# Optimization experiments

Measured on AMD Instinct MI355X. Metric: run time of the kernel, lower is better.

The kernel has to match this reference:

```python
import jax, jax.numpy as jnp
import numpy as np

B, U, I, H = 1024, 8, 512, 512


def setup_inputs() -> dict:
    key = jax.random.key(0)
    ks = jax.random.split(key, 6)
    s_i = 1.0 / np.sqrt(H)  # torch GRU init: U(-1/sqrt(H), 1/sqrt(H))
    inputs = jax.random.normal(ks[0], (B, U, I), dtype=jnp.float32)
    hidden = jax.random.normal(ks[1], (B, U, H), dtype=jnp.float32)
    W_ih = jax.random.uniform(ks[2], (U, 3 * H, I), minval=-s_i, maxval=s_i, dtype=jnp.float32)
    W_hh = jax.random.uniform(ks[3], (U, 3 * H, H), minval=-s_i, maxval=s_i, dtype=jnp.float32)
    b_ih = jax.random.uniform(ks[4], (U, 3 * H), minval=-s_i, maxval=s_i, dtype=jnp.float32)
    b_hh = jax.random.uniform(ks[5], (U, 3 * H), minval=-s_i, maxval=s_i, dtype=jnp.float32)
    return {"inputs": inputs, "hidden": hidden, "W_ih": W_ih, "W_hh": W_hh, "b_ih": b_ih, "b_hh": b_hh}


def reference(inputs, hidden, W_ih, W_hh, b_ih, b_hh):
    # Grouped single-step GRU: all num_units cells computed in one batched matmul pair.
    # gx, gh: [B, U, 3H]
    gx = jnp.einsum('bui,ugi->bug', inputs, W_ih) + b_ih[None]
    gh = jnp.einsum('buh,ugh->bug', hidden, W_hh) + b_hh[None]
    xr, xz, xn = jnp.split(gx, 3, axis=-1)
    hr, hz, hn = jnp.split(gh, 3, axis=-1)
    r = jax.nn.sigmoid(xr + hr)
    z = jax.nn.sigmoid(xz + hz)
    n = jnp.tanh(xn + r * hn)
    return (1.0 - z) * n + z * hidden
```

## Files before the change

### kernel.cpp

```cpp
#include <hip/hip_runtime.h>
#include <hip/hip_bf16.h>
#include <stdint.h>


#define B_ 1024
#define U_ 8
#define I_ 512
#define H_ 512
#define KDIM 512

#define NX (B_ * U_ * I_)
#define NW (U_ * 3 * H_ * I_)
#define OFF_X 0
#define OFF_H NX
#define OFF_WIH (2 * NX)
#define OFF_WHH (2 * NX + NW)
#define NTOT (2 * NX + 2 * NW)
#define WS_NEED ((size_t)NTOT * 2)

#define BM 64
#define BN 64
#define BK 32
#define NITER (KDIM / BK)
#define SLAB_B 4096
#define BUF_B (8 * SLAB_B)
#define ESTR 68

typedef __attribute__((ext_vector_type(8))) short short8;
typedef __attribute__((ext_vector_type(4))) float floatx4;

__device__ __forceinline__ unsigned int pk2bf(float a, float b) {
    float2 f2; f2.x = a; f2.y = b;
    union { __hip_bfloat162 h; unsigned int u; } cv;
    cv.h = __float22bfloat162_rn(f2);
    return cv.u;
}

__device__ __forceinline__ void async16(const void* g, void* l) {
    __builtin_amdgcn_global_load_lds(
        (const __attribute__((address_space(1))) void*)g,
        (__attribute__((address_space(3))) void*)l, 16, 0, 0);
}

__global__ __launch_bounds__(256)
void convert_bf16_kernel(const float* __restrict__ x, const float* __restrict__ h,
                         const float* __restrict__ wih, const float* __restrict__ whh,
                         unsigned short* __restrict__ ws)
{
    const size_t base = ((size_t)blockIdx.x * 256 + threadIdx.x) * 8;
    const float* src; size_t off;
    if (base < (size_t)OFF_H)        { src = x;   off = OFF_X; }
    else if (base < (size_t)OFF_WIH) { src = h;   off = OFF_H; }
    else if (base < (size_t)OFF_WHH) { src = wih; off = OFF_WIH; }
    else                             { src = whh; off = OFF_WHH; }
    const float4 v0 = *(const float4*)(src + (base - off));
    const float4 v1 = *(const float4*)(src + (base - off) + 4);
    uint4 o;
    o.x = pk2bf(v0.x, v0.y);
    o.y = pk2bf(v0.z, v0.w);
    o.z = pk2bf(v1.x, v1.y);
    o.w = pk2bf(v1.z, v1.w);
    *(uint4*)(ws + base) = o;
}

union Smem {
    char raw[2 * BUF_B];
    float ep[3][BM * ESTR];
};

__global__ __launch_bounds__(512, 4)
void gru_main_kernel(const unsigned short* __restrict__ ws,
                     const float* __restrict__ hidden,
                     const float* __restrict__ b_ih,
                     const float* __restrict__ b_hh,
                     float* __restrict__ out)
{
    const int u  = blockIdx.x >> 3;
    const int nb = blockIdx.x & 7;
    const int mb = blockIdx.y;
    const int b0 = mb * BM;
    const int h0 = nb * BN;

    const int tid  = threadIdx.x;
    const int lane = tid & 63;
    const int wave = tid >> 6;
    const int lr   = lane & 15;
    const int q    = lane >> 4;
    const int wm   = wave & 1;
    const int wn   = (wave >> 1) & 1;
    const int g2   = wave >> 2;

    __shared__ Smem smem;

    const unsigned short* gbase; int grstr;
    if (wave == 0)      { gbase = ws + OFF_X + ((size_t)b0 * U_ + u) * I_; grstr = U_ * I_; }
    else if (wave == 1) { gbase = ws + OFF_H + ((size_t)b0 * U_ + u) * H_; grstr = U_ * H_; }
    else if (wave <= 4) { int g = wave - 2; gbase = ws + OFF_WIH + ((size_t)(u * 3 + g) * H_ + h0) * I_; grstr = I_; }
    else                { int g = wave - 5; gbase = ws + OFF_WHH + ((size_t)(u * 3 + g) * H_ + h0) * H_; grstr = H_; }

    const unsigned short* gptr[4];
    int ldsoff[4];
    #pragma unroll
    for (int i = 0; i < 4; ++i) {
        const int line = i * 8 + (lane >> 3);
        const int pos  = (lane & 7) ^ (line & 7);
        const int row  = 2 * line + (pos >> 2);
        const int ch   = pos & 3;
        gptr[i]   = gbase + (size_t)row * grstr + ch * 8;
        ldsoff[i] = wave * SLAB_B + i * 1024 + lane * 16;
    }

    int aoff[2], boff[2];
    #pragma unroll
    for (int t = 0; t < 2; ++t) {
        {
            const int r = wm * 32 + t * 16 + lr;
            const int line = r >> 1;
            const int pp = (((r & 1) * 4 + q)) ^ (line & 7);
            aoff[t] = line * 128 + pp * 16;
        }
        {
            const int r = wn * 32 + t * 16 + lr;
            const int line = r >> 1;
            const int pp = (((r & 1) * 4 + q)) ^ (line & 7);
            boff[t] = line * 128 + pp * 16;
        }
    }

    floatx4 acc[3][2][2];
    #pragma unroll
    for (int g = 0; g < 3; ++g)
        #pragma unroll
        for (int mt = 0; mt < 2; ++mt)
            #pragma unroll
            for (int nt = 0; nt < 2; ++nt)
                acc[g][mt][nt] = (floatx4){0.f, 0.f, 0.f, 0.f};

    const int aslab = g2;
    const int bbase = 2 + 3 * g2;

    #pragma unroll
    for (int i = 0; i < 4; ++i) {
        async16(gptr[i], smem.raw + ldsoff[i]);
        gptr[i] += BK;
    }

    for (int it = 0; it < NITER; ++it) {
        const int cur = it & 1;
        __syncthreads();

        if (it + 1 < NITER) {
            const int nxtoff = ((it + 1) & 1) * BUF_B;
            #pragma unroll
            for (int i = 0; i < 4; ++i) {
                async16(gptr[i], smem.raw + nxtoff + ldsoff[i]);
                gptr[i] += BK;
            }
        }

        const char* base = smem.raw + cur * BUF_B;
        const short8 a0 = *(const short8*)(base + aslab * SLAB_B + aoff[0]);
        const short8 a1 = *(const short8*)(base + aslab * SLAB_B + aoff[1]);
        #pragma unroll
        for (int g = 0; g < 3; ++g) {
            const char* bslab = base + (bbase + g) * SLAB_B;
            #pragma unroll
            for (int nt = 0; nt < 2; ++nt) {
                const short8 bf = *(const short8*)(bslab + boff[nt]);
                acc[g][0][nt] = __builtin_amdgcn_mfma_f32_16x16x32_bf16(a0, bf, acc[g][0][nt], 0, 0, 0);
                acc[g][1][nt] = __builtin_amdgcn_mfma_f32_16x16x32_bf16(a1, bf, acc[g][1][nt], 0, 0, 0);
            }
        }
    }
    __syncthreads();

    const float* bih = b_ih + u * (3 * H_);
    const float* bhh = b_hh + u * (3 * H_);

    if (g2 == 1) {
        #pragma unroll
        for (int nt = 0; nt < 2; ++nt) {
            const int col = wn * 32 + nt * 16 + lr;
            const float bhr = bhh[h0 + col];
            const float bhz = bhh[H_ + h0 + col];
            const float bhn = bhh[2 * H_ + h0 + col];
            #pragma unroll
            for (int mt = 0; mt < 2; ++mt)
                #pragma unroll
                for (int r = 0; r < 4; ++r) {
                    const int row = wm * 32 + mt * 16 + q * 4 + r;
                    smem.ep[0][row * ESTR + col] = acc[0][mt][nt][r] + bhr;
                    smem.ep[1][row * ESTR + col] = acc[1][mt][nt][r] + bhz;
                    smem.ep[2][row * ESTR + col] = acc[2][mt][nt][r] + bhn;
                }
        }
    }
    __syncthreads();

    if (g2 == 0) {
        #pragma unroll
        for (int nt = 0; nt < 2; ++nt) {
            const int col  = wn * 32 + nt * 16 + lr;
            const int hcol = h0 + col;
            const float bir  = bih[hcol];
            const float biz  = bih[H_ + hcol];
            const float bin_ = bih[2 * H_ + hcol];
            #pragma unroll
            for (int mt = 0; mt < 2; ++mt)
                #pragma unroll
                for (int r = 0; r < 4; ++r) {
                    const int row  = wm * 32 + mt * 16 + q * 4 + r;
                    const size_t gidx = ((size_t)(b0 + row) * U_ + u) * H_ + hcol;
                    const float hprev = hidden[gidx];
                    const float hr = smem.ep[0][row * ESTR + col];
                    const float hz = smem.ep[1][row * ESTR + col];
                    const float hn = smem.ep[2][row * ESTR + col];
                    const float xr = acc[0][mt][nt][r] + bir;
                    const float xz = acc[1][mt][nt][r] + biz;
                    const float xn = acc[2][mt][nt][r] + bin_;
                    const float rg = 1.f / (1.f + __expf(-(xr + hr)));
                    const float zg = 1.f / (1.f + __expf(-(xz + hz)));
                    const float ng = tanhf(xn + rg * hn);
                    out[gidx] = (1.f - zg) * ng + zg * hprev;
                }
        }
    }
}

#define LSTR 40
union SmemF {
    short bf[8][BM * LSTR];
    float ep[3][BM * ESTR];
};

__global__ __launch_bounds__(512, 4)
void gru_fallback_kernel(const float* __restrict__ inputs, const float* __restrict__ hidden,
                         const float* __restrict__ W_ih, const float* __restrict__ W_hh,
                         const float* __restrict__ b_ih, const float* __restrict__ b_hh,
                         float* __restrict__ out)
{
    const int nb = blockIdx.x;
    const int mb = blockIdx.y;
    const int u  = blockIdx.z;
    const int b0 = mb * BM, h0 = nb * BN;
    const int tid = threadIdx.x, lane = tid & 63, wave = tid >> 6;
    const int lr = lane & 15, q = lane >> 4;
    const int wm = wave & 1, wn = (wave >> 1) & 1, g2 = wave >> 2;

    __shared__ SmemF smem;

    const float* srcs[8]; int rstr[8];
    srcs[0] = inputs + ((size_t)b0 * U_ + u) * I_;         rstr[0] = U_ * I_;
    srcs[1] = hidden + ((size_t)b0 * U_ + u) * H_;         rstr[1] = U_ * H_;
    srcs[2] = W_ih + ((size_t)(u * 3 + 0) * H_ + h0) * I_; rstr[2] = I_;
    srcs[3] = W_ih + ((size_t)(u * 3 + 1) * H_ + h0) * I_; rstr[3] = I_;
    srcs[4] = W_ih + ((size_t)(u * 3 + 2) * H_ + h0) * I_; rstr[4] = I_;
    srcs[5] = W_hh + ((size_t)(u * 3 + 0) * H_ + h0) * H_; rstr[5] = H_;
    srcs[6] = W_hh + ((size_t)(u * 3 + 1) * H_ + h0) * H_; rstr[6] = H_;
    srcs[7] = W_hh + ((size_t)(u * 3 + 2) * H_ + h0) * H_; rstr[7] = H_;

    const int srow = tid >> 3, c4 = (tid & 7) * 4;
    const float* tb[8];
    #pragma unroll
    for (int s = 0; s < 8; ++s) tb[s] = srcs[s] + (size_t)srow * rstr[s] + c4;

    floatx4 acc[3][2][2];
    #pragma unroll
    for (int g = 0; g < 3; ++g)
        #pragma unroll
        for (int mt = 0; mt < 2; ++mt)
            #pragma unroll
            for (int nt = 0; nt < 2; ++nt) acc[g][mt][nt] = (floatx4){0.f, 0.f, 0.f, 0.f};

    const int aslab = g2, bbase = 2 + 3 * g2;
    float4 pre[8];
    #pragma unroll
    for (int s = 0; s < 8; ++s) pre[s] = *(const float4*)(tb[s]);

    for (int k0 = 0; k0 < KDIM; k0 += 32) {
        #pragma unroll
        for (int s = 0; s < 8; ++s) {
            uint2 w; w.x = pk2bf(pre[s].x, pre[s].y); w.y = pk2bf(pre[s].z, pre[s].w);
            *(uint2*)&smem.bf[s][srow * LSTR + c4] = w;
        }
        __syncthreads();
        if (k0 + 32 < KDIM) {
            #pragma unroll
            for (int s = 0; s < 8; ++s) pre[s] = *(const float4*)(tb[s] + k0 + 32);
        }
        short8 afr[2];
        #pragma unroll
        for (int mt = 0; mt < 2; ++mt)
            afr[mt] = *(const short8*)&smem.bf[aslab][(wm * 32 + mt * 16 + lr) * LSTR + q * 8];
        #pragma unroll
        for (int g = 0; g < 3; ++g) {
            const short8 bf0 = *(const short8*)&smem.bf[bbase + g][(wn * 32 + lr) * LSTR + q * 8];
            const short8 bf1 = *(const short8*)&smem.bf[bbase + g][(wn * 32 + 16 + lr) * LSTR + q * 8];
            #pragma unroll
            for (int mt = 0; mt < 2; ++mt) {
                acc[g][mt][0] = __builtin_amdgcn_mfma_f32_16x16x32_bf16(afr[mt], bf0, acc[g][mt][0], 0, 0, 0);
                acc[g][mt][1] = __builtin_amdgcn_mfma_f32_16x16x32_bf16(afr[mt], bf1, acc[g][mt][1], 0, 0, 0);
            }
        }
        __syncthreads();
    }

    const float* bih = b_ih + u * (3 * H_);
    const float* bhh = b_hh + u * (3 * H_);
    if (g2 == 1) {
        #pragma unroll
        for (int nt = 0; nt < 2; ++nt) {
            const int col = wn * 32 + nt * 16 + lr;
            const float bhr = bhh[h0 + col], bhz = bhh[H_ + h0 + col], bhn = bhh[2 * H_ + h0 + col];
            #pragma unroll
            for (int mt = 0; mt < 2; ++mt)
                #pragma unroll
                for (int r = 0; r < 4; ++r) {
                    const int row = wm * 32 + mt * 16 + q * 4 + r;
                    smem.ep[0][row * ESTR + col] = acc[0][mt][nt][r] + bhr;
                    smem.ep[1][row * ESTR + col] = acc[1][mt][nt][r] + bhz;
                    smem.ep[2][row * ESTR + col] = acc[2][mt][nt][r] + bhn;
                }
        }
    }
    __syncthreads();
    if (g2 == 0) {
        #pragma unroll
        for (int nt = 0; nt < 2; ++nt) {
            const int col = wn * 32 + nt * 16 + lr, hcol = h0 + col;
            const float bir = bih[hcol], biz = bih[H_ + hcol], bin_ = bih[2 * H_ + hcol];
            #pragma unroll
            for (int mt = 0; mt < 2; ++mt)
                #pragma unroll
                for (int r = 0; r < 4; ++r) {
                    const int row = wm * 32 + mt * 16 + q * 4 + r;
                    const size_t gidx = ((size_t)(b0 + row) * U_ + u) * H_ + hcol;
                    const float hprev = hidden[gidx];
                    const float hr = smem.ep[0][row * ESTR + col];
                    const float hz = smem.ep[1][row * ESTR + col];
                    const float hn = smem.ep[2][row * ESTR + col];
                    const float xr = acc[0][mt][nt][r] + bir;
                    const float xz = acc[1][mt][nt][r] + biz;
                    const float xn = acc[2][mt][nt][r] + bin_;
                    const float rg = 1.f / (1.f + __expf(-(xr + hr)));
                    const float zg = 1.f / (1.f + __expf(-(xz + hz)));
                    const float ng = tanhf(xn + rg * hn);
                    out[gidx] = (1.f - zg) * ng + zg * hprev;
                }
        }
    }
}

extern "C" void kernel_launch(void* const* d_in, const int* in_sizes, int n_in,
                              void* d_out, int out_size, void* d_ws, size_t ws_size,
                              hipStream_t stream) {
    const float* inputs = (const float*)d_in[0];
    const float* hidden = (const float*)d_in[1];
    const float* W_ih   = (const float*)d_in[2];
    const float* W_hh   = (const float*)d_in[3];
    const float* b_ih   = (const float*)d_in[4];
    const float* b_hh   = (const float*)d_in[5];
    float* out = (float*)d_out;

    if (ws_size >= WS_NEED) {
        unsigned short* ws = (unsigned short*)d_ws;
        convert_bf16_kernel<<<NTOT / 2048, 256, 0, stream>>>(inputs, hidden, W_ih, W_hh, ws);
        dim3 grid(64, 16, 1);
        gru_main_kernel<<<grid, 512, 0, stream>>>(ws, hidden, b_ih, b_hh, out);
    } else {
        dim3 grid(8, 16, 8);
        gru_fallback_kernel<<<grid, 512, 0, stream>>>(inputs, hidden, W_ih, W_hh, b_ih, b_hh, out);
    }
}
```

Before: 175.4 us.

## Double batch tile to 128 rows and stream epilogue through LDS in chunks

The batch tile grows from 64 to 128 rows, so each block reuses the six weight slabs across twice as many rows and loads them half as often. The load assignment is rebalanced to 5 async copies per wave, and each wave now holds 4x2 accumulator tiles per gate. The epilogue exchanges the hidden-gate partials through LDS in four m-chunks of float4 writes, which keeps the shared buffer small. The cost is more registers per thread, which may lower occupancy, and a grid half the size (512 blocks), which may leave CUs underused.

```diff
diff --git a/kernel.cpp b/kernel.cpp
--- a/kernel.cpp
+++ b/kernel.cpp
@@ -18,12 +18,11 @@
 #define NTOT (2 * NX + 2 * NW)
 #define WS_NEED ((size_t)NTOT * 2)
 
-#define BM 64
+#define BM 128
 #define BN 64
 #define BK 32
 #define NITER (KDIM / BK)
-#define SLAB_B 4096
-#define BUF_B (8 * SLAB_B)
+#define BUF_B 40960
 #define ESTR 68
 
 typedef __attribute__((ext_vector_type(8))) short short8;
@@ -63,11 +62,6 @@
     *(uint4*)(ws + base) = o;
 }
 
-union Smem {
-    char raw[2 * BUF_B];
-    float ep[3][BM * ESTR];
-};
-
 __global__ __launch_bounds__(512, 4)
 void gru_main_kernel(const unsigned short* __restrict__ ws,
                      const float* __restrict__ hidden,
@@ -86,62 +80,68 @@
     const int wave = tid >> 6;
     const int lr   = lane & 15;
     const int q    = lane >> 4;
-    const int wm   = wave & 1;
-    const int wn   = (wave >> 1) & 1;
+    const int p    = wave & 3;
+    const int wm   = p & 1;
+    const int wn   = p >> 1;
     const int g2   = wave >> 2;
 
-    __shared__ Smem smem;
-
-    const unsigned short* gbase; int grstr;
-    if (wave == 0)      { gbase = ws + OFF_X + ((size_t)b0 * U_ + u) * I_; grstr = U_ * I_; }
-    else if (wave == 1) { gbase = ws + OFF_H + ((size_t)b0 * U_ + u) * H_; grstr = U_ * H_; }
-    else if (wave <= 4) { int g = wave - 2; gbase = ws + OFF_WIH + ((size_t)(u * 3 + g) * H_ + h0) * I_; grstr = I_; }
-    else                { int g = wave - 5; gbase = ws + OFF_WHH + ((size_t)(u * 3 + g) * H_ + h0) * H_; grstr = H_; }
-
-    const unsigned short* gptr[4];
-    int ldsoff[4];
-    #pragma unroll
-    for (int i = 0; i < 4; ++i) {
-        const int line = i * 8 + (lane >> 3);
+    __shared__ __align__(16) char smem[2 * BUF_B];
+
+    const unsigned short* baseX = ws + OFF_X + ((size_t)b0 * U_ + u) * I_;
+    const unsigned short* baseH = ws + OFF_H + ((size_t)b0 * U_ + u) * H_;
+    const unsigned short* wb[6];
+    #pragma unroll
+    for (int w = 0; w < 3; ++w) {
+        wb[w]     = ws + OFF_WIH + ((size_t)(u * 3 + w) * H_ + h0) * I_;
+        wb[w + 3] = ws + OFF_WHH + ((size_t)(u * 3 + w) * H_ + h0) * H_;
+    }
+
+    const unsigned short* gptr[5];
+    int ldsoff[5];
+    #pragma unroll
+    for (int i = 0; i < 5; ++i) {
+        const int j = wave * 5 + i;
+        const unsigned short* sbase; int rstr, group, soff;
+        if (j < 8)       { sbase = baseX;          rstr = U_ * I_; group = j;            soff = 0; }
+        else if (j < 16) { sbase = baseH;          rstr = U_ * H_; group = j - 8;        soff = 8192; }
+        else             { const int w = (j - 16) >> 2;
+                           sbase = wb[w];          rstr = I_;      group = (j - 16) & 3; soff = 16384 + w * 4096; }
+        const int line = group * 8 + (lane >> 3);
         const int pos  = (lane & 7) ^ (line & 7);
         const int row  = 2 * line + (pos >> 2);
         const int ch   = pos & 3;
-        gptr[i]   = gbase + (size_t)row * grstr + ch * 8;
-        ldsoff[i] = wave * SLAB_B + i * 1024 + lane * 16;
-    }
-
-    int aoff[2], boff[2];
-    #pragma unroll
-    for (int t = 0; t < 2; ++t) {
-        {
-            const int r = wm * 32 + t * 16 + lr;
-            const int line = r >> 1;
-            const int pp = (((r & 1) * 4 + q)) ^ (line & 7);
-            aoff[t] = line * 128 + pp * 16;
-        }
-        {
-            const int r = wn * 32 + t * 16 + lr;
-            const int line = r >> 1;
-            const int pp = (((r & 1) * 4 + q)) ^ (line & 7);
-            boff[t] = line * 128 + pp * 16;
-        }
-    }
-
-    floatx4 acc[3][2][2];
+        gptr[i]   = sbase + (size_t)row * rstr + ch * 8;
+        ldsoff[i] = soff + group * 1024 + lane * 16;
+    }
+
+    int aoff[4], boff[2];
+    #pragma unroll
+    for (int mt = 0; mt < 4; ++mt) {
+        const int r = wm * 64 + mt * 16 + lr;
+        const int line = r >> 1;
+        const int pp = (((r & 1) * 4 + q)) ^ (line & 7);
+        aoff[mt] = line * 128 + pp * 16;
+    }
+    #pragma unroll
+    for (int nt = 0; nt < 2; ++nt) {
+        const int r = wn * 32 + nt * 16 + lr;
+        const int line = r >> 1;
+        const int pp = (((r & 1) * 4 + q)) ^ (line & 7);
+        boff[nt] = line * 128 + pp * 16;
+    }
+
+    floatx4 acc[3][4][2];
     #pragma unroll
     for (int g = 0; g < 3; ++g)
         #pragma unroll
-        for (int mt = 0; mt < 2; ++mt)
+        for (int mt = 0; mt < 4; ++mt)
             #pragma unroll
             for (int nt = 0; nt < 2; ++nt)
                 acc[g][mt][nt] = (floatx4){0.f, 0.f, 0.f, 0.f};
 
-    const int aslab = g2;
-    const int bbase = 2 + 3 * g2;
-
-    #pragma unroll
-    for (int i = 0; i < 4; ++i) {
-        async16(gptr[i], smem.raw + ldsoff[i]);
+    #pragma unroll
+    for (int i = 0; i < 5; ++i) {
+        async16(gptr[i], smem + ldsoff[i]);
         gptr[i] += BK;
     }
 
@@ -150,87 +150,87 @@
         __syncthreads();
 
         if (it + 1 < NITER) {
-            const int nxtoff = ((it + 1) & 1) * BUF_B;
-            #pragma unroll
-            for (int i = 0; i < 4; ++i) {
-                async16(gptr[i], smem.raw + nxtoff + ldsoff[i]);
+            const int nxt = ((it + 1) & 1) * BUF_B;
+            #pragma unroll
+            for (int i = 0; i < 5; ++i) {
+                async16(gptr[i], smem + nxt + ldsoff[i]);
                 gptr[i] += BK;
             }
         }
 
-        const char* base = smem.raw + cur * BUF_B;
-        const short8 a0 = *(const short8*)(base + aslab * SLAB_B + aoff[0]);
-        const short8 a1 = *(const short8*)(base + aslab * SLAB_B + aoff[1]);
+        const char* base  = smem + cur * BUF_B;
+        const char* abase = base + g2 * 8192;
+        short8 a[4];
+        #pragma unroll
+        for (int mt = 0; mt < 4; ++mt)
+            a[mt] = *(const short8*)(abase + aoff[mt]);
         #pragma unroll
         for (int g = 0; g < 3; ++g) {
-            const char* bslab = base + (bbase + g) * SLAB_B;
+            const char* bslab = base + 16384 + (g2 * 3 + g) * 4096;
             #pragma unroll
             for (int nt = 0; nt < 2; ++nt) {
                 const short8 bf = *(const short8*)(bslab + boff[nt]);
-                acc[g][0][nt] = __builtin_amdgcn_mfma_f32_16x16x32_bf16(a0, bf, acc[g][0][nt], 0, 0, 0);
-                acc[g][1][nt] = __builtin_amdgcn_mfma_f32_16x16x32_bf16(a1, bf, acc[g][1][nt], 0, 0, 0);
+                #pragma unroll
+                for (int mt = 0; mt < 4; ++mt)
+                    acc[g][mt][nt] = __builtin_amdgcn_mfma_f32_16x16x32_bf16(
+                        a[mt], bf, acc[g][mt][nt], 0, 0, 0);
             }
         }
     }
-    __syncthreads();
-
+
+    float4* ep = (float4*)smem;
     const float* bih = b_ih + u * (3 * H_);
     const float* bhh = b_hh + u * (3 * H_);
 
-    if (g2 == 1) {
-        #pragma unroll
-        for (int nt = 0; nt < 2; ++nt) {
-            const int col = wn * 32 + nt * 16 + lr;
-            const float bhr = bhh[h0 + col];
-            const float bhz = bhh[H_ + h0 + col];
-            const float bhn = bhh[2 * H_ + h0 + col];
-            #pragma unroll
-            for (int mt = 0; mt < 2; ++mt)
+    for (int m = 0; m < 4; ++m) {
+        __syncthreads();
+        if (g2 == 1) {
+            #pragma unroll
+            for (int g = 0; g < 3; ++g)
+                #pragma unroll
+                for (int nt = 0; nt < 2; ++nt)
+                    ep[((g * 2 + nt) * 4 + p) * 64 + lane] =
+                        (float4){acc[g][m][nt][0], acc[g][m][nt][1],
+                                 acc[g][m][nt][2], acc[g][m][nt][3]};
+        }
+        __syncthreads();
+        if (g2 == 0) {
+            #pragma unroll
+            for (int nt = 0; nt < 2; ++nt) {
+                const int col  = wn * 32 + nt * 16 + lr;
+                const int hcol = h0 + col;
+                const float bir  = bih[hcol],          bhr = bhh[hcol];
+                const float biz  = bih[H_ + hcol],     bhz = bhh[H_ + hcol];
+                const float bin_ = bih[2 * H_ + hcol], bhn = bhh[2 * H_ + hcol];
+                const float4 hrv = ep[((0 * 2 + nt) * 4 + p) * 64 + lane];
+                const float4 hzv = ep[((1 * 2 + nt) * 4 + p) * 64 + lane];
+                const float4 hnv = ep[((2 * 2 + nt) * 4 + p) * 64 + lane];
                 #pragma unroll
                 for (int r = 0; r < 4; ++r) {
-                    const int row = wm * 32 + mt * 16 + q * 4 + r;
-                    smem.ep[0][row * ESTR + col] = acc[0][mt][nt][r] + bhr;
-                    smem.ep[1][row * ESTR + col] = acc[1][mt][nt][r] + bhz;
-                    smem.ep[2][row * ESTR + col] = acc[2][mt][nt][r] + bhn;
-                }
-        }
-    }
-    __syncthreads();
-
-    if (g2 == 0) {
-        #pragma unroll
-        for (int nt = 0; nt < 2; ++nt) {
-            const int col  = wn * 32 + nt * 16 + lr;
-            const int hcol = h0 + col;
-            const float bir  = bih[hcol];
-            const float biz  = bih[H_ + hcol];
-            const float bin_ = bih[2 * H_ + hcol];
-            #pragma unroll
-            for (int mt = 0; mt < 2; ++mt)
-                #pragma unroll
-                for (int r = 0; r < 4; ++r) {
-                    const int row  = wm * 32 + mt * 16 + q * 4 + r;
+                    const int row = wm * 64 + m * 16 + q * 4 + r;
                     const size_t gidx = ((size_t)(b0 + row) * U_ + u) * H_ + hcol;
                     const float hprev = hidden[gidx];
-                    const float hr = smem.ep[0][row * ESTR + col];
-                    const float hz = smem.ep[1][row * ESTR + col];
-                    const float hn = smem.ep[2][row * ESTR + col];
-                    const float xr = acc[0][mt][nt][r] + bir;
-                    const float xz = acc[1][mt][nt][r] + biz;
-                    const float xn = acc[2][mt][nt][r] + bin_;
+                    const float hr = (r == 0 ? hrv.x : r == 1 ? hrv.y : r == 2 ? hrv.z : hrv.w) + bhr;
+                    const float hz = (r == 0 ? hzv.x : r == 1 ? hzv.y : r == 2 ? hzv.z : hzv.w) + bhz;
+                    const float hn = (r == 0 ? hnv.x : r == 1 ? hnv.y : r == 2 ? hnv.z : hnv.w) + bhn;
+                    const float xr = acc[0][m][nt][r] + bir;
+                    const float xz = acc[1][m][nt][r] + biz;
+                    const float xn = acc[2][m][nt][r] + bin_;
                     const float rg = 1.f / (1.f + __expf(-(xr + hr)));
                     const float zg = 1.f / (1.f + __expf(-(xz + hz)));
                     const float ng = tanhf(xn + rg * hn);
                     out[gidx] = (1.f - zg) * ng + zg * hprev;
                 }
+            }
         }
     }
 }
 
 #define LSTR 40
+#define FBM 64
 union SmemF {
-    short bf[8][BM * LSTR];
-    float ep[3][BM * ESTR];
+    short bf[8][FBM * LSTR];
+    float ep[3][FBM * ESTR];
 };
 
 __global__ __launch_bounds__(512, 4)
@@ -242,7 +242,7 @@
     const int nb = blockIdx.x;
     const int mb = blockIdx.y;
     const int u  = blockIdx.z;
-    const int b0 = mb * BM, h0 = nb * BN;
+    const int b0 = mb * FBM, h0 = nb * BN;
     const int tid = threadIdx.x, lane = tid & 63, wave = tid >> 6;
     const int lr = lane & 15, q = lane >> 4;
     const int wm = wave & 1, wn = (wave >> 1) & 1, g2 = wave >> 2;
@@ -365,7 +365,7 @@
     if (ws_size >= WS_NEED) {
         unsigned short* ws = (unsigned short*)d_ws;
         convert_bf16_kernel<<<NTOT / 2048, 256, 0, stream>>>(inputs, hidden, W_ih, W_hh, ws);
-        dim3 grid(64, 16, 1);
+        dim3 grid(64, 8, 1);
         gru_main_kernel<<<grid, 512, 0, stream>>>(ws, hidden, b_ih, b_hh, out);
     } else {
         dim3 grid(8, 16, 8);
```

New measurement: 236.9 us. 1.35x slower.
